# Performance work log

Hardware: AMD Instinct MI355X
Metric: run time of the kernel (lower is better)

The kernel has to match this reference:

```python
import jax, jax.numpy as jnp
import numpy as np

B, D_IN, D_S = 16384, 1024, 1024


def setup_inputs() -> dict:
    key = jax.random.key(0)
    ks = jax.random.split(key, 7)
    s_in = 1.0 / np.sqrt(D_IN)
    s_h = 1.0 / np.sqrt(D_S)
    return {
        "input": jax.random.normal(ks[0], (B, D_IN), jnp.float32),
        "cell_state": jax.random.normal(ks[1], (B, D_S), jnp.float32),
        "hidden_state": jax.random.normal(ks[2], (B, D_S), jnp.float32),
        "Wx": jax.random.uniform(ks[3], (4, D_S, D_IN), jnp.float32, -s_in, s_in),
        "bx": jax.random.uniform(ks[4], (4, D_S), jnp.float32, -s_in, s_in),
        "Wh": jax.random.uniform(ks[5], (4, D_S, D_S), jnp.float32, -s_h, s_h),
        "bh": jax.random.uniform(ks[6], (4, D_S), jnp.float32, -s_h, s_h),
    }


def reference(input, cell_state, hidden_state, Wx, bx, Wh, bh):
    # Fused: two batched GEMMs produce all 4 gate pre-activations.
    # gates_x, gates_h: [4, B, D_S]; gate order: forget, input, cand, output
    gx = jnp.einsum('bi,gsi->gbs', input, Wx) + bx[:, None, :]
    gh = jnp.einsum('bh,gsh->gbs', hidden_state, Wh) + bh[:, None, :]
    pre = gx + gh
    f = jax.nn.sigmoid(pre[0])
    i = jax.nn.sigmoid(pre[1]) * jnp.tanh(pre[2])
    new_cell_state = cell_state * f + i
    output = jnp.tanh(new_cell_state) * jax.nn.sigmoid(pre[3])
    return (new_cell_state, output)
```

## Files before the change

kernel.cpp:

```cpp
#include <hip/hip_runtime.h>
#include <hip/hip_bf16.h>
#include <stdint.h>


typedef short bf16x8 __attribute__((ext_vector_type(8)));
typedef float f32x4 __attribute__((ext_vector_type(4)));

#define B_ROWS 16384
#define D_K 2048

__device__ __forceinline__ unsigned short f2bf(float f) {
    unsigned u = __builtin_bit_cast(unsigned, f);
    u += 0x7FFFu + ((u >> 16) & 1u);
    return (unsigned short)(u >> 16);
}

__device__ __forceinline__ float sigf(float x) { return 1.0f / (1.0f + __expf(-x)); }
__device__ __forceinline__ float tanhfast(float x) { return 2.0f / (1.0f + __expf(-2.0f * x)) - 1.0f; }

#define GLD16(gp, lp)                                                          \
    __builtin_amdgcn_global_load_lds(                                          \
        (const __attribute__((address_space(1))) unsigned int*)(gp),           \
        (__attribute__((address_space(3))) unsigned int*)(lp), 16, 0, 0)


__global__ void pack_A_kernel(const float* __restrict__ x,
                              const float* __restrict__ h,
                              unsigned short* __restrict__ A) {
    const int total = B_ROWS * (D_K / 4);
    for (int v = blockIdx.x * blockDim.x + threadIdx.x; v < total;
         v += gridDim.x * blockDim.x) {
        const int b = v >> 9;
        const int k0 = (v & 511) << 2;
        const float* src = (k0 < 1024) ? (x + (size_t)b * 1024 + k0)
                                       : (h + (size_t)b * 1024 + (k0 - 1024));
        float4 f = *(const float4*)src;
        unsigned p0 = (unsigned)f2bf(f.x) | ((unsigned)f2bf(f.y) << 16);
        unsigned p1 = (unsigned)f2bf(f.z) | ((unsigned)f2bf(f.w) << 16);
        uint2 o; o.x = p0; o.y = p1;
        *(uint2*)(A + (size_t)v * 4) = o;
    }
}

__global__ void pack_W_kernel(const float* __restrict__ Wx,
                              const float* __restrict__ Wh,
                              unsigned short* __restrict__ W) {
    const int total = 4096 * (D_K / 4);
    for (int v = blockIdx.x * blockDim.x + threadIdx.x; v < total;
         v += gridDim.x * blockDim.x) {
        const int n = v >> 9;
        const int k0 = (v & 511) << 2;
        const float* src = (k0 < 1024) ? (Wx + (size_t)n * 1024 + k0)
                                       : (Wh + (size_t)n * 1024 + (k0 - 1024));
        float4 f = *(const float4*)src;
        unsigned p0 = (unsigned)f2bf(f.x) | ((unsigned)f2bf(f.y) << 16);
        unsigned p1 = (unsigned)f2bf(f.z) | ((unsigned)f2bf(f.w) << 16);
        uint2 o; o.x = p0; o.y = p1;
        *(uint2*)(W + (size_t)v * 4) = o;
    }
}

__global__ void pack_bias_kernel(const float* __restrict__ bx,
                                 const float* __restrict__ bh,
                                 float* __restrict__ bias) {
    int i = blockIdx.x * blockDim.x + threadIdx.x;
    if (i < 4096) bias[i] = bx[i] + bh[i];
}


__global__ __launch_bounds__(512, 2) void lstm_gemm_kernel(
    const unsigned short* __restrict__ A,
    const unsigned short* __restrict__ W,
    const float* __restrict__ bias,
    const float* __restrict__ cell,
    float* __restrict__ out) {
    __shared__ __align__(16) unsigned short smem[2][32768];

    const int bid = blockIdx.x;
    const int wg = (bid & 7) * 128 + (bid >> 3);
    const int brow = (wg >> 4) << 8;
    const int bcol = (wg & 15) << 6;

    const int tid = threadIdx.x;
    const int wid = tid >> 6;
    const int lane = tid & 63;
    const int wr = wid >> 1, wc = wid & 1;
    const int lr = lane & 15, lg = lane >> 4;
    const int l8 = lane >> 3;
    const int lcol = (((lane & 7) ^ l8) << 3);

    f32x4 acc[4][4][2];
#pragma unroll
    for (int g = 0; g < 4; ++g)
#pragma unroll
        for (int m = 0; m < 4; ++m)
#pragma unroll
            for (int n = 0; n < 2; ++n) acc[g][m][n] = (f32x4){0.f, 0.f, 0.f, 0.f};

    const unsigned short* gp[8];
#pragma unroll
    for (int i = 0; i < 8; ++i) {
        const int c = wid * 8 + i;
        if (c < 32) {
            gp[i] = A + (size_t)(brow + c * 8 + l8) * D_K + lcol;
        } else {
            const int cw = c - 32;
            gp[i] = W + (size_t)((cw >> 3) * 1024 + bcol + (cw & 7) * 8 + l8) * D_K + lcol;
        }
    }

    char* const lds0 = (char*)smem + (size_t)wid * 8 * 1024;

#define STAGE(buf, kt)                                                         \
    do {                                                                       \
        char* _d = lds0 + (size_t)(buf) * 65536;                               \
        _Pragma("unroll")                                                      \
        for (int _i = 0; _i < 8; ++_i)                                         \
            GLD16(gp[_i] + (kt), _d + _i * 1024);                              \
    } while (0)

#define COMPUTE(buf)                                                           \
    do {                                                                       \
        const unsigned short* _sA = smem[buf];                                 \
        const unsigned short* _sW = smem[buf] + 16384;                         \
        _Pragma("unroll")                                                      \
        for (int kk = 0; kk < 2; ++kk) {                                       \
            const int swk = (kk * 32 + lg * 8) ^ ((lr & 7) << 3);              \
            bf16x8 a[4];                                                       \
            _Pragma("unroll")                                                  \
            for (int m = 0; m < 4; ++m)                                        \
                a[m] = *(const bf16x8*)&_sA[(wr * 64 + m * 16 + lr) * 64 + swk]; \
            _Pragma("unroll")                                                  \
            for (int g = 0; g < 4; ++g) {                                      \
                const int wbase = (g * 64 + wc * 32 + lr) * 64 + swk;          \
                bf16x8 w0 = *(const bf16x8*)&_sW[wbase];                       \
                bf16x8 w1 = *(const bf16x8*)&_sW[wbase + 16 * 64];             \
                _Pragma("unroll")                                              \
                for (int m = 0; m < 4; ++m) {                                  \
                    acc[g][m][0] = __builtin_amdgcn_mfma_f32_16x16x32_bf16(    \
                        a[m], w0, acc[g][m][0], 0, 0, 0);                      \
                    acc[g][m][1] = __builtin_amdgcn_mfma_f32_16x16x32_bf16(    \
                        a[m], w1, acc[g][m][1], 0, 0, 0);                      \
                }                                                              \
            }                                                                  \
        }                                                                      \
    } while (0)

    STAGE(0, 0);

    int cur = 0;
    for (int t = 0; t < 31; ++t) {
        STAGE(cur ^ 1, (t + 1) * 64);
        asm volatile("s_waitcnt vmcnt(8)" ::: "memory");
        __builtin_amdgcn_s_barrier();
        asm volatile("" ::: "memory");
        COMPUTE(cur);
        asm volatile("" ::: "memory");
        __builtin_amdgcn_s_barrier();
        asm volatile("" ::: "memory");
        cur ^= 1;
    }
    asm volatile("s_waitcnt vmcnt(0)" ::: "memory");
    __builtin_amdgcn_s_barrier();
    asm volatile("" ::: "memory");
    COMPUTE(cur);

#undef STAGE
#undef COMPUTE

    float bv[4][2];
#pragma unroll
    for (int g = 0; g < 4; ++g)
#pragma unroll
        for (int n = 0; n < 2; ++n)
            bv[g][n] = bias[(g << 10) + bcol + wc * 32 + n * 16 + lr];

    float* outc = out;
    float* outh = out + (size_t)B_ROWS * 1024;
#pragma unroll
    for (int m = 0; m < 4; ++m) {
#pragma unroll
        for (int r = 0; r < 4; ++r) {
            const int b = brow + wr * 64 + m * 16 + lg * 4 + r;
            const size_t base = (size_t)b * 1024 + bcol + wc * 32;
#pragma unroll
            for (int n = 0; n < 2; ++n) {
                const int so = n * 16 + lr;
                float pf = acc[0][m][n][r] + bv[0][n];
                float pi = acc[1][m][n][r] + bv[1][n];
                float pc = acc[2][m][n][r] + bv[2][n];
                float po = acc[3][m][n][r] + bv[3][n];
                float cl = cell[base + so];
                float nc = cl * sigf(pf) + sigf(pi) * tanhfast(pc);
                outc[base + so] = nc;
                outh[base + so] = tanhfast(nc) * sigf(po);
            }
        }
    }
}


__global__ void lstm_naive_kernel(const float* __restrict__ x,
                                  const float* __restrict__ cell,
                                  const float* __restrict__ h,
                                  const float* __restrict__ Wx,
                                  const float* __restrict__ bx,
                                  const float* __restrict__ Wh,
                                  const float* __restrict__ bh,
                                  float* __restrict__ out) {
    int idx = blockIdx.x * blockDim.x + threadIdx.x;
    if (idx >= B_ROWS * 1024) return;
    int b = idx >> 10, s = idx & 1023;
    const float* xr = x + (size_t)b * 1024;
    const float* hr = h + (size_t)b * 1024;
    float pre[4];
#pragma unroll
    for (int g = 0; g < 4; ++g) {
        float acc = bx[(g << 10) + s] + bh[(g << 10) + s];
        const float* wx = Wx + ((size_t)(g << 10) + s) * 1024;
        const float* wh = Wh + ((size_t)(g << 10) + s) * 1024;
        for (int k = 0; k < 1024; ++k) acc += xr[k] * wx[k] + hr[k] * wh[k];
        pre[g] = acc;
    }
    float nc = cell[idx] * sigf(pre[0]) + sigf(pre[1]) * tanhfast(pre[2]);
    out[idx] = nc;
    out[(size_t)B_ROWS * 1024 + idx] = tanhfast(nc) * sigf(pre[3]);
}


extern "C" void kernel_launch(void* const* d_in, const int* in_sizes, int n_in,
                              void* d_out, int out_size, void* d_ws, size_t ws_size,
                              hipStream_t stream) {
    const float* x    = (const float*)d_in[0];
    const float* cell = (const float*)d_in[1];
    const float* hid  = (const float*)d_in[2];
    const float* Wx   = (const float*)d_in[3];
    const float* bx   = (const float*)d_in[4];
    const float* Wh   = (const float*)d_in[5];
    const float* bh   = (const float*)d_in[6];
    float* out = (float*)d_out;

    const size_t szA = (size_t)B_ROWS * D_K * 2;
    const size_t szW = (size_t)4096 * D_K * 2;
    const size_t szB = 4096 * 4;
    if (ws_size < szA + szW + szB) {
        lstm_naive_kernel<<<(B_ROWS * 1024) / 256, 256, 0, stream>>>(
            x, cell, hid, Wx, bx, Wh, bh, out);
        return;
    }

    unsigned short* Ab = (unsigned short*)d_ws;
    unsigned short* Wb = (unsigned short*)((char*)d_ws + szA);
    float* bias = (float*)((char*)d_ws + szA + szW);

    pack_A_kernel<<<8192, 256, 0, stream>>>(x, hid, Ab);
    pack_W_kernel<<<2048, 256, 0, stream>>>(Wx, Wh, Wb);
    pack_bias_kernel<<<16, 256, 0, stream>>>(bx, bh, bias);

    lstm_gemm_kernel<<<1024, 512, 0, stream>>>(Ab, Wb, bias, cell, out);
}
```

Baseline: 315.8 us.

## Switch GEMM to 4-stage K=32 LDS ring with single barrier per step

The pipeline moves from a double-buffered K=64 tile with two barriers per iteration to a 4-deep ring of K=32 tiles with one barrier per step, so loads run two stages ahead. The warp layout changes from 4x2 to 2x4, each wave now owns 128 rows by 16 columns, and the XOR swizzle is replaced by a 16-row chunk layout. s_setprio is raised around the MFMA block, and the tile-to-block mapping now iterates over rows first. It aims to hide global latency and cut barrier overhead, at the risk of more LDS bank conflicts from the unswizzled layout and fewer MFMAs per barrier.

Result: slower. 338.5 us (+7.2%).

```diff
diff --git a/kernel.cpp b/kernel.cpp
--- a/kernel.cpp
+++ b/kernel.cpp
@@ -22,6 +22,8 @@
     __builtin_amdgcn_global_load_lds(                                          \
         (const __attribute__((address_space(1))) unsigned int*)(gp),           \
         (__attribute__((address_space(3))) unsigned int*)(lp), 16, 0, 0)
+
+#define FENCE() asm volatile("" ::: "memory")
 
 
 __global__ void pack_A_kernel(const float* __restrict__ x,
@@ -74,127 +76,112 @@
     const float* __restrict__ bias,
     const float* __restrict__ cell,
     float* __restrict__ out) {
-    __shared__ __align__(16) unsigned short smem[2][32768];
+    __shared__ __align__(16) unsigned short smem[4][16384];
 
     const int bid = blockIdx.x;
-    const int wg = (bid & 7) * 128 + (bid >> 3);
-    const int brow = (wg >> 4) << 8;
-    const int bcol = (wg & 15) << 6;
+    const int wgi = (bid & 7) * 128 + (bid >> 3);
+    const int brow = (wgi & 63) << 8;
+    const int bcol = (wgi >> 6) << 6;
 
     const int tid = threadIdx.x;
     const int wid = tid >> 6;
     const int lane = tid & 63;
-    const int wr = wid >> 1, wc = wid & 1;
+    const int wr = wid >> 2;
+    const int wc = wid & 3;
     const int lr = lane & 15, lg = lane >> 4;
-    const int l8 = lane >> 3;
-    const int lcol = (((lane & 7) ^ l8) << 3);
-
-    f32x4 acc[4][4][2];
+    const int l16 = lane >> 2;
+    const int lk = (lane & 3) << 3;
+
+    f32x4 acc[4][8];
 #pragma unroll
     for (int g = 0; g < 4; ++g)
 #pragma unroll
-        for (int m = 0; m < 4; ++m)
-#pragma unroll
-            for (int n = 0; n < 2; ++n) acc[g][m][n] = (f32x4){0.f, 0.f, 0.f, 0.f};
-
-    const unsigned short* gp[8];
-#pragma unroll
-    for (int i = 0; i < 8; ++i) {
-        const int c = wid * 8 + i;
-        if (c < 32) {
-            gp[i] = A + (size_t)(brow + c * 8 + l8) * D_K + lcol;
+        for (int m = 0; m < 8; ++m) acc[g][m] = (f32x4){0.f, 0.f, 0.f, 0.f};
+
+    const unsigned short* gp[4];
+#pragma unroll
+    for (int i = 0; i < 4; ++i) {
+        const int c = wid * 4 + i;
+        if (c < 16) {
+            gp[i] = A + (size_t)(brow + c * 16 + l16) * D_K + lk;
         } else {
-            const int cw = c - 32;
-            gp[i] = W + (size_t)((cw >> 3) * 1024 + bcol + (cw & 7) * 8 + l8) * D_K + lcol;
+            const int cw = c - 16;
+            gp[i] = W + (size_t)((cw >> 2) * 1024 + bcol + (cw & 3) * 16 + l16) * D_K + lk;
         }
     }
-
-    char* const lds0 = (char*)smem + (size_t)wid * 8 * 1024;
 
 #define STAGE(buf, kt)                                                         \
     do {                                                                       \
-        char* _d = lds0 + (size_t)(buf) * 65536;                               \
-        _Pragma("unroll")                                                      \
-        for (int _i = 0; _i < 8; ++_i)                                         \
-            GLD16(gp[_i] + (kt), _d + _i * 1024);                              \
+        char* _d = (char*)smem[buf] + (wid * 4) * 1024;                        \
+        _Pragma("unroll")                                                      \
+        for (int _i = 0; _i < 4; ++_i) GLD16(gp[_i] + (kt), _d + _i * 1024);   \
     } while (0)
 
 #define COMPUTE(buf)                                                           \
     do {                                                                       \
-        const unsigned short* _sA = smem[buf];                                 \
-        const unsigned short* _sW = smem[buf] + 16384;                         \
-        _Pragma("unroll")                                                      \
-        for (int kk = 0; kk < 2; ++kk) {                                       \
-            const int swk = (kk * 32 + lg * 8) ^ ((lr & 7) << 3);              \
-            bf16x8 a[4];                                                       \
+        const unsigned short* _sb = smem[buf];                                 \
+        bf16x8 a[8], w[4];                                                     \
+        _Pragma("unroll")                                                      \
+        for (int m = 0; m < 8; ++m)                                            \
+            a[m] = *(const bf16x8*)&_sb[(wr * 8 + m) * 512 + lr * 32 + lg * 8]; \
+        _Pragma("unroll")                                                      \
+        for (int g = 0; g < 4; ++g)                                            \
+            w[g] = *(const bf16x8*)&_sb[8192 + (g * 4 + wc) * 512 + lr * 32 + lg * 8]; \
+        __builtin_amdgcn_s_setprio(1);                                         \
+        _Pragma("unroll")                                                      \
+        for (int g = 0; g < 4; ++g) {                                          \
             _Pragma("unroll")                                                  \
-            for (int m = 0; m < 4; ++m)                                        \
-                a[m] = *(const bf16x8*)&_sA[(wr * 64 + m * 16 + lr) * 64 + swk]; \
-            _Pragma("unroll")                                                  \
-            for (int g = 0; g < 4; ++g) {                                      \
-                const int wbase = (g * 64 + wc * 32 + lr) * 64 + swk;          \
-                bf16x8 w0 = *(const bf16x8*)&_sW[wbase];                       \
-                bf16x8 w1 = *(const bf16x8*)&_sW[wbase + 16 * 64];             \
-                _Pragma("unroll")                                              \
-                for (int m = 0; m < 4; ++m) {                                  \
-                    acc[g][m][0] = __builtin_amdgcn_mfma_f32_16x16x32_bf16(    \
-                        a[m], w0, acc[g][m][0], 0, 0, 0);                      \
-                    acc[g][m][1] = __builtin_amdgcn_mfma_f32_16x16x32_bf16(    \
-                        a[m], w1, acc[g][m][1], 0, 0, 0);                      \
-                }                                                              \
-            }                                                                  \
+            for (int m = 0; m < 8; ++m)                                        \
+                acc[g][m] = __builtin_amdgcn_mfma_f32_16x16x32_bf16(           \
+                    a[m], w[g], acc[g][m], 0, 0, 0);                           \
         }                                                                      \
+        __builtin_amdgcn_s_setprio(0);                                         \
     } while (0)
 
     STAGE(0, 0);
-
-    int cur = 0;
-    for (int t = 0; t < 31; ++t) {
-        STAGE(cur ^ 1, (t + 1) * 64);
-        asm volatile("s_waitcnt vmcnt(8)" ::: "memory");
+    STAGE(1, 32);
+
+    for (int t = 0; t < 62; ++t) {
+        STAGE((t + 2) & 3, (t + 2) * 32);
+        asm volatile("s_waitcnt vmcnt(6)" ::: "memory");
         __builtin_amdgcn_s_barrier();
-        asm volatile("" ::: "memory");
-        COMPUTE(cur);
-        asm volatile("" ::: "memory");
-        __builtin_amdgcn_s_barrier();
-        asm volatile("" ::: "memory");
-        cur ^= 1;
-    }
+        FENCE();
+        COMPUTE(t & 3);
+        FENCE();
+    }
+    asm volatile("s_waitcnt vmcnt(4)" ::: "memory");
+    __builtin_amdgcn_s_barrier();
+    FENCE();
+    COMPUTE(2);
+    FENCE();
     asm volatile("s_waitcnt vmcnt(0)" ::: "memory");
     __builtin_amdgcn_s_barrier();
-    asm volatile("" ::: "memory");
-    COMPUTE(cur);
+    FENCE();
+    COMPUTE(3);
 
 #undef STAGE
 #undef COMPUTE
 
-    float bv[4][2];
-#pragma unroll
-    for (int g = 0; g < 4; ++g)
-#pragma unroll
-        for (int n = 0; n < 2; ++n)
-            bv[g][n] = bias[(g << 10) + bcol + wc * 32 + n * 16 + lr];
+    float bv[4];
+#pragma unroll
+    for (int g = 0; g < 4; ++g) bv[g] = bias[(g << 10) + bcol + wc * 16 + lr];
 
     float* outc = out;
     float* outh = out + (size_t)B_ROWS * 1024;
 #pragma unroll
-    for (int m = 0; m < 4; ++m) {
+    for (int m = 0; m < 8; ++m) {
 #pragma unroll
         for (int r = 0; r < 4; ++r) {
-            const int b = brow + wr * 64 + m * 16 + lg * 4 + r;
-            const size_t base = (size_t)b * 1024 + bcol + wc * 32;
-#pragma unroll
-            for (int n = 0; n < 2; ++n) {
-                const int so = n * 16 + lr;
-                float pf = acc[0][m][n][r] + bv[0][n];
-                float pi = acc[1][m][n][r] + bv[1][n];
-                float pc = acc[2][m][n][r] + bv[2][n];
-                float po = acc[3][m][n][r] + bv[3][n];
-                float cl = cell[base + so];
-                float nc = cl * sigf(pf) + sigf(pi) * tanhfast(pc);
-                outc[base + so] = nc;
-                outh[base + so] = tanhfast(nc) * sigf(po);
-            }
+            const int b = brow + wr * 128 + m * 16 + lg * 4 + r;
+            const size_t idx = (size_t)b * 1024 + bcol + wc * 16 + lr;
+            float pf = acc[0][m][r] + bv[0];
+            float pi = acc[1][m][r] + bv[1];
+            float pc = acc[2][m][r] + bv[2];
+            float po = acc[3][m][r] + bv[3];
+            float cl = cell[idx];
+            float nc = cl * sigf(pf) + sigf(pi) * tanhfast(pc);
+            outc[idx] = nc;
+            outh[idx] = tanhfast(nc) * sigf(po);
         }
     }
 }
```
